# Performance work log

Measured on AMD Instinct MI355X. Metric: run time of the kernel, lower is better.

Reference implementation:

```python
import jax, jax.numpy as jnp
import numpy as np
import math

T = 0.28
EPS = 1e-06
D_MODEL = 1024
N_HEADS = 16
D_K = D_MODEL // N_HEADS


def compute_radius(t, epsilon):
    raw = math.sqrt(4.0 * t * math.log(1.0 / epsilon))
    return max(int(math.ceil(raw * 2.0)), 1)

RADIUS = compute_radius(T, EPS)  # = 8 for t=0.28, eps=1e-6
WIN = RADIUS + 1                 # causal band window: j in [i-RADIUS, i]


def setup_inputs() -> dict:
    key = jax.random.key(0)
    ks = jax.random.split(key, 5)
    B, S = 2, 4096
    x = jax.random.normal(ks[0], (B, S, D_MODEL), dtype=jnp.float32)
    scale = 1.0 / math.sqrt(D_MODEL)
    Wq = jax.random.normal(ks[1], (D_MODEL, D_MODEL), dtype=jnp.float32) * scale
    Wk = jax.random.normal(ks[2], (D_MODEL, D_MODEL), dtype=jnp.float32) * scale
    Wv = jax.random.normal(ks[3], (D_MODEL, D_MODEL), dtype=jnp.float32) * scale
    Wo = jax.random.normal(ks[4], (D_MODEL, D_MODEL), dtype=jnp.float32) * scale
    return {"x": x, "Wq": Wq, "Wk": Wk, "Wv": Wv, "Wo": Wo}


def reference(x, Wq, Wk, Wv, Wo):
    B, S, _ = x.shape

    def split_heads(h):  # (B,S,D) -> (B,H,S,dk)
        return h.reshape(B, S, N_HEADS, D_K).transpose(0, 2, 1, 3)

    q = split_heads(x @ Wq)
    k = split_heads(x @ Wk)
    v = split_heads(x @ Wv)

    # Banded causal attention: token i attends to j in [i-RADIUS, i].
    # This equals the full masked softmax in the torch reference because
    # all out-of-band / non-causal entries are -inf there.
    pos = jnp.arange(S)
    idx = pos[:, None] + jnp.arange(-RADIUS, 1)[None, :]
    valid = idx >= 0                                       # left boundary
    idx_c = jnp.clip(idx, 0, S - 1)

    k_win = k[:, :, idx_c, :]
    v_win = v[:, :, idx_c, :]

    scores = jnp.einsum('bhsd,bhswd->bhsw', q, k_win) / (2.0 * T)
    scores = jnp.where(valid[None, None, :, :], scores, -jnp.inf)
    wts = jax.nn.softmax(scores, axis=-1)
    wts = jnp.nan_to_num(wts, nan=0.0)  # diagonal always valid, but keep parity

    attn = jnp.einsum('bhsw,bhswd->bhsd', wts, v_win)      # (B,H,S,dk)
    attn = attn.transpose(0, 2, 1, 3).reshape(B, S, D_MODEL)
    return attn @ Wo
```

## Files before the change

### kernel.cpp

```cpp
#include <hip/hip_runtime.h>
#include <stdint.h>

constexpr int S_LEN = 4096;
constexpr int DM    = 1024;
constexpr int RAD   = 8;
constexpr float INV2T = 1.7857142857142858f;

constexpr int BM = 128, BN = 128, BK = 64;

typedef _Float16 h8v __attribute__((ext_vector_type(8)));
typedef float f32x4  __attribute__((ext_vector_type(4)));

static __device__ __forceinline__ void gl_lds16(const void* gp, void* lp) {
  auto g = (const __attribute__((address_space(1))) void*)(uintptr_t)gp;
  auto l = (__attribute__((address_space(3))) void*)(uint32_t)(uintptr_t)lp;
  __builtin_amdgcn_global_load_lds(g, l, 16, 0, 0);
}

__global__ __launch_bounds__(256) void sda_cast_kernel(const float* __restrict__ X,
                                                       _Float16* __restrict__ Y) {
  int i = blockIdx.x * 256 + threadIdx.x;
  const float4* x4 = (const float4*)X;
  float4 a = x4[2 * i], b = x4[2 * i + 1];
  float f[8] = {a.x, a.y, a.z, a.w, b.x, b.y, b.z, b.w};
  union { _Float16 h[8]; uint4 v; } o;
#pragma unroll
  for (int j = 0; j < 8; ++j) o.h[j] = (_Float16)f[j];
  ((uint4*)Y)[i] = o.v;
}

__global__ __launch_bounds__(256) void sda_transcast_kernel(
    const float* __restrict__ W0, const float* __restrict__ W1,
    const float* __restrict__ W2, const float* __restrict__ W3,
    _Float16* __restrict__ T0, _Float16* __restrict__ T1,
    _Float16* __restrict__ T2, _Float16* __restrict__ T3) {
  __shared__ float t[32][33];
  const float* W = blockIdx.z == 0 ? W0 : (blockIdx.z == 1 ? W1 : (blockIdx.z == 2 ? W2 : W3));
  _Float16*    T = blockIdx.z == 0 ? T0 : (blockIdx.z == 1 ? T1 : (blockIdx.z == 2 ? T2 : T3));
  int tx = threadIdx.x, ty = threadIdx.y;
  int n0 = blockIdx.x * 32, k0 = blockIdx.y * 32;
#pragma unroll
  for (int i = 0; i < 4; ++i)
    t[ty + 8 * i][tx] = W[(size_t)(k0 + ty + 8 * i) * DM + n0 + tx];
  __syncthreads();
#pragma unroll
  for (int i = 0; i < 4; ++i)
    T[(size_t)(n0 + ty + 8 * i) * DM + k0 + tx] = (_Float16)t[tx][ty + 8 * i];
}

template <bool OUTF16>
__global__ __launch_bounds__(256) void sda_gemm_swz_kernel(
    const _Float16* __restrict__ A, const _Float16* __restrict__ Bt,
    void* __restrict__ C0, void* __restrict__ C1, void* __restrict__ C2) {
  constexpr int Kd = DM;
  __shared__ __align__(16) _Float16 As[BM * BK];
  __shared__ __align__(16) _Float16 Bs[BN * BK];

  int blk = blockIdx.x;
  int xcd = blk & 7, slot = blk >> 3;
  int xt = slot >> 3, ys = slot & 7;
  int yt = (xcd << 3) | ys;
  int m0 = yt * BM, n0 = xt * BN;

  int tid = threadIdx.x, wid = tid >> 6, lane = tid & 63;
  int srow = lane >> 3;
  int sgk = ((lane & 7) ^ (srow & 7)) * 8;
  int wm = (wid >> 1) * 64, wn = (wid & 1) * 64;
  int fm = lane & 15, fc = lane >> 4;

  f32x4 acc[4][4] = {};

  for (int kt = 0; kt < Kd / BK; ++kt) {
    if (kt) __syncthreads();
    int kk = kt * BK;
    int r0 = wid * 32;
#pragma unroll
    for (int i = 0; i < 4; ++i) {
      gl_lds16(A  + (size_t)(m0 + r0 + i * 8 + srow) * Kd + kk + sgk, &As[(r0 + i * 8) * BK]);
      gl_lds16(Bt + (size_t)(n0 + r0 + i * 8 + srow) * Kd + kk + sgk, &Bs[(r0 + i * 8) * BK]);
    }
    __syncthreads();

#pragma unroll
    for (int ks = 0; ks < 2; ++ks) {
      h8v af[4], bfr[4];
#pragma unroll
      for (int i = 0; i < 4; ++i) {
        int row = wm + i * 16 + fm;
        af[i] = *(const h8v*)&As[row * BK + (((ks * 4 + fc) ^ (row & 7)) * 8)];
      }
#pragma unroll
      for (int j = 0; j < 4; ++j) {
        int row = wn + j * 16 + fm;
        bfr[j] = *(const h8v*)&Bs[row * BK + (((ks * 4 + fc) ^ (row & 7)) * 8)];
      }
#pragma unroll
      for (int i = 0; i < 4; ++i)
#pragma unroll
        for (int j = 0; j < 4; ++j)
          acc[i][j] = __builtin_amdgcn_mfma_f32_16x16x32_f16(af[i], bfr[j], acc[i][j], 0, 0, 0);
    }
  }

  int which = n0 >> 10, nc = n0 & 1023;
  void* Cv = which == 0 ? C0 : (which == 1 ? C1 : C2);

  int rr = (lane >> 4) * 4, cc = lane & 15;
#pragma unroll
  for (int i = 0; i < 4; ++i)
#pragma unroll
    for (int j = 0; j < 4; ++j) {
      size_t base = (size_t)(m0 + wm + i * 16 + rr) * DM + (nc + wn + j * 16 + cc);
#pragma unroll
      for (int r = 0; r < 4; ++r) {
        float v = acc[i][j][r];
        if constexpr (OUTF16) ((_Float16*)Cv)[base + (size_t)r * DM] = (_Float16)v;
        else                  ((float*)Cv)[base + (size_t)r * DM] = v;
      }
    }
}

__global__ __launch_bounds__(256) void sda_attn_kernel(
    const _Float16* __restrict__ Q, const _Float16* __restrict__ K,
    const _Float16* __restrict__ V, _Float16* __restrict__ O) {
  constexpr int VS  = 68;
  __shared__ __align__(16) _Float16 qs[64 * 64];
  __shared__ __align__(16) _Float16 ks[80 * 64];
  __shared__ __align__(16) _Float16 vs[96 * VS];
  __shared__ __align__(16) float    scb[4 * 16 * 33];
  __shared__ __align__(16) _Float16 wts[64 * 96];

  int bh = blockIdx.y, b = bh >> 4, h = bh & 15;
  int s0 = blockIdx.x * 64;
  int tid = threadIdx.x;
  size_t headoff = (size_t)b * S_LEN * DM + h * 64;

  for (int idx = tid; idx < 64 * 8; idx += 256) {
    int row = idx >> 3, ch = (idx & 7) * 8;
    *(uint4*)&qs[row * 64 + ch] =
        *(const uint4*)(Q + headoff + (size_t)(s0 + row) * DM + ch);
  }
  for (int idx = tid; idx < 72 * 8; idx += 256) {
    int row = idx >> 3, ch = (idx & 7) * 8;
    int pos = s0 - RAD + row;
    uint4 kv = make_uint4(0, 0, 0, 0), vv = make_uint4(0, 0, 0, 0);
    if (pos >= 0) {
      size_t off = headoff + (size_t)pos * DM + ch;
      kv = *(const uint4*)(K + off);
      vv = *(const uint4*)(V + off);
    }
    *(uint4*)&ks[row * 64 + ch] = kv;
    *(uint2*)&vs[row * VS + ch]     = make_uint2(vv.x, vv.y);
    *(uint2*)&vs[row * VS + ch + 4] = make_uint2(vv.z, vv.w);
  }
  if (tid < 64)
    *(uint4*)&ks[(72 + (tid >> 3)) * 64 + (tid & 7) * 8] = make_uint4(0, 0, 0, 0);
  for (int idx = tid; idx < 24 * 17; idx += 256) {
    int row = 72 + idx / 17, c = (idx % 17) * 4;
    *(uint2*)&vs[row * VS + c] = make_uint2(0, 0);
  }
  for (int idx = tid; idx < 768; idx += 256)
    ((uint4*)wts)[idx] = make_uint4(0, 0, 0, 0);
  __syncthreads();

  int wid = tid >> 6, lane = tid & 63;
  int fm = lane & 15, fkg = (lane >> 4) * 8;
  int rr = (lane >> 4) * 4, cc = lane & 15;

  {
    f32x4 accs[2] = {};
    h8v aq0 = *(const h8v*)&qs[(wid * 16 + fm) * 64 + fkg];
    h8v aq1 = *(const h8v*)&qs[(wid * 16 + fm) * 64 + 32 + fkg];
#pragma unroll
    for (int ti = 0; ti < 2; ++ti) {
      int t = wid + ti;
      h8v bk0 = *(const h8v*)&ks[(t * 16 + fm) * 64 + fkg];
      h8v bk1 = *(const h8v*)&ks[(t * 16 + fm) * 64 + 32 + fkg];
      accs[ti] = __builtin_amdgcn_mfma_f32_16x16x32_f16(aq0, bk0, accs[ti], 0, 0, 0);
      accs[ti] = __builtin_amdgcn_mfma_f32_16x16x32_f16(aq1, bk1, accs[ti], 0, 0, 0);
    }
#pragma unroll
    for (int ti = 0; ti < 2; ++ti)
#pragma unroll
      for (int r = 0; r < 4; ++r)
        scb[wid * 528 + (rr + r) * 33 + ti * 16 + cc] = accs[ti][r];
  }
  __syncthreads();

  if (tid < 64) {
    int r = tid, s = s0 + r;
    const float* my = &scb[(r >> 4) * 528 + (r & 15) * 33 + (r & 15)];
    float e[9], mx = -1e30f;
#pragma unroll
    for (int j = 0; j < 9; ++j) {
      float p = my[j] * INV2T;
      e[j] = (s - RAD + j >= 0) ? p : -1e30f;
      mx = fmaxf(mx, e[j]);
    }
    float se = 0.f;
#pragma unroll
    for (int j = 0; j < 9; ++j) { e[j] = __expf(e[j] - mx); se += e[j]; }
    float inv = 1.f / se;
#pragma unroll
    for (int j = 0; j < 9; ++j)
      wts[r * 96 + r + j] = (_Float16)(e[j] * inv);
  }
  __syncthreads();

  f32x4 acco[4] = {};
#pragma unroll
  for (int step = 0; step < 3; ++step) {
    h8v aw = *(const h8v*)&wts[(wid * 16 + fm) * 96 + step * 32 + fkg];
    int kb = step * 32 + fkg;
#pragma unroll
    for (int t = 0; t < 4; ++t) {
      h8v bv;
#pragma unroll
      for (int j = 0; j < 8; ++j)
        bv[j] = vs[(kb + j) * VS + t * 16 + fm];
      acco[t] = __builtin_amdgcn_mfma_f32_16x16x32_f16(aw, bv, acco[t], 0, 0, 0);
    }
  }
#pragma unroll
  for (int t = 0; t < 4; ++t)
#pragma unroll
    for (int r = 0; r < 4; ++r)
      O[headoff + (size_t)(s0 + wid * 16 + rr + r) * DM + t * 16 + cc] =
          (_Float16)acco[t][r];
}

extern "C" void kernel_launch(void* const* d_in, const int* in_sizes, int n_in,
                              void* d_out, int out_size, void* d_ws, size_t ws_size,
                              hipStream_t stream) {
  (void)in_sizes; (void)n_in; (void)out_size; (void)ws_size;
  const float* x  = (const float*)d_in[0];
  const float* Wq = (const float*)d_in[1];
  const float* Wk = (const float*)d_in[2];
  const float* Wv = (const float*)d_in[3];
  const float* Wo = (const float*)d_in[4];

  char* ws = (char*)d_ws;
  const size_t MB = 1ull << 20;
  _Float16* xh    = (_Float16*)(ws + 0);
  _Float16* WqkvT = (_Float16*)(ws + 16 * MB);
  _Float16* WoT   = (_Float16*)(ws + 22 * MB);
  _Float16* Qh    = (_Float16*)(ws + 24 * MB);
  _Float16* Kh    = (_Float16*)(ws + 40 * MB);
  _Float16* Vh    = (_Float16*)(ws + 56 * MB);
  _Float16* Ah    = (_Float16*)(ws + 72 * MB);

  sda_cast_kernel<<<4096, 256, 0, stream>>>(x, xh);
  sda_transcast_kernel<<<dim3(32, 32, 4), dim3(32, 8), 0, stream>>>(
      Wq, Wk, Wv, Wo,
      WqkvT, WqkvT + (size_t)DM * DM, WqkvT + 2ull * DM * DM, WoT);

  sda_gemm_swz_kernel<true><<<1536, 256, 0, stream>>>(xh, WqkvT, Qh, Kh, Vh);
  sda_attn_kernel<<<dim3(64, 32), 256, 0, stream>>>(Qh, Kh, Vh, Ah);
  sda_gemm_swz_kernel<false><<<512, 256, 0, stream>>>(Ah, WoT, d_out, d_out, d_out);
}
```

Baseline: 190.2 us.

## Fuse prep kernels, narrow Wo GEMM tiles, transpose V in attention LDS

Merges the x cast and the weight transpose-cast into one launch, which saves a kernel launch. Adds a dedicated output-projection GEMM with 128x64 tiles so it runs 1024 blocks instead of 512, giving better CU occupancy on the smaller problem. In the attention kernel, Q fragments are loaded straight from global into registers instead of going through LDS, and V is stored transposed so the PV MFMA operand becomes one vector LDS read instead of eight scalar reads. The risks are smaller tiles lowering data reuse in the Wo GEMM and bank conflicts from the scalar transposed V stores.

```diff
diff --git a/kernel.cpp b/kernel.cpp
--- a/kernel.cpp
+++ b/kernel.cpp
@@ -17,41 +17,43 @@
   __builtin_amdgcn_global_load_lds(g, l, 16, 0, 0);
 }
 
-__global__ __launch_bounds__(256) void sda_cast_kernel(const float* __restrict__ X,
-                                                       _Float16* __restrict__ Y) {
-  int i = blockIdx.x * 256 + threadIdx.x;
-  const float4* x4 = (const float4*)X;
-  float4 a = x4[2 * i], b = x4[2 * i + 1];
-  float f[8] = {a.x, a.y, a.z, a.w, b.x, b.y, b.z, b.w};
-  union { _Float16 h[8]; uint4 v; } o;
-#pragma unroll
-  for (int j = 0; j < 8; ++j) o.h[j] = (_Float16)f[j];
-  ((uint4*)Y)[i] = o.v;
-}
-
-__global__ __launch_bounds__(256) void sda_transcast_kernel(
+__global__ __launch_bounds__(256) void sda_prep_kernel(
+    const float* __restrict__ X, _Float16* __restrict__ XH,
     const float* __restrict__ W0, const float* __restrict__ W1,
     const float* __restrict__ W2, const float* __restrict__ W3,
     _Float16* __restrict__ T0, _Float16* __restrict__ T1,
     _Float16* __restrict__ T2, _Float16* __restrict__ T3) {
   __shared__ float t[32][33];
-  const float* W = blockIdx.z == 0 ? W0 : (blockIdx.z == 1 ? W1 : (blockIdx.z == 2 ? W2 : W3));
-  _Float16*    T = blockIdx.z == 0 ? T0 : (blockIdx.z == 1 ? T1 : (blockIdx.z == 2 ? T2 : T3));
+  int z = blockIdx.z;
   int tx = threadIdx.x, ty = threadIdx.y;
-  int n0 = blockIdx.x * 32, k0 = blockIdx.y * 32;
-#pragma unroll
-  for (int i = 0; i < 4; ++i)
-    t[ty + 8 * i][tx] = W[(size_t)(k0 + ty + 8 * i) * DM + n0 + tx];
-  __syncthreads();
-#pragma unroll
-  for (int i = 0; i < 4; ++i)
-    T[(size_t)(n0 + ty + 8 * i) * DM + k0 + tx] = (_Float16)t[tx][ty + 8 * i];
-}
-
-template <bool OUTF16>
+  if (z < 4) {
+    const float* W = z == 0 ? W0 : (z == 1 ? W1 : (z == 2 ? W2 : W3));
+    _Float16*    T = z == 0 ? T0 : (z == 1 ? T1 : (z == 2 ? T2 : T3));
+    int n0 = blockIdx.x * 32, k0 = blockIdx.y * 32;
+#pragma unroll
+    for (int i = 0; i < 4; ++i)
+      t[ty + 8 * i][tx] = W[(size_t)(k0 + ty + 8 * i) * DM + n0 + tx];
+    __syncthreads();
+#pragma unroll
+    for (int i = 0; i < 4; ++i)
+      T[(size_t)(n0 + ty + 8 * i) * DM + k0 + tx] = (_Float16)t[tx][ty + 8 * i];
+  } else {
+    int blk = (z - 4) * 1024 + blockIdx.y * 32 + blockIdx.x;
+    int i = blk * 256 + ty * 32 + tx;
+    const float4* x4 = (const float4*)X;
+    float4 a = x4[2 * i], b = x4[2 * i + 1];
+    float f[8] = {a.x, a.y, a.z, a.w, b.x, b.y, b.z, b.w};
+    union { _Float16 h[8]; uint4 v; } o;
+#pragma unroll
+    for (int j = 0; j < 8; ++j) o.h[j] = (_Float16)f[j];
+    ((uint4*)XH)[i] = o.v;
+  }
+}
+
 __global__ __launch_bounds__(256) void sda_gemm_swz_kernel(
     const _Float16* __restrict__ A, const _Float16* __restrict__ Bt,
-    void* __restrict__ C0, void* __restrict__ C1, void* __restrict__ C2) {
+    _Float16* __restrict__ C0, _Float16* __restrict__ C1,
+    _Float16* __restrict__ C2) {
   constexpr int Kd = DM;
   __shared__ __align__(16) _Float16 As[BM * BK];
   __shared__ __align__(16) _Float16 Bs[BN * BK];
@@ -103,7 +105,7 @@
   }
 
   int which = n0 >> 10, nc = n0 & 1023;
-  void* Cv = which == 0 ? C0 : (which == 1 ? C1 : C2);
+  _Float16* Cv = which == 0 ? C0 : (which == 1 ? C1 : C2);
 
   int rr = (lane >> 4) * 4, cc = lane & 15;
 #pragma unroll
@@ -112,21 +114,84 @@
     for (int j = 0; j < 4; ++j) {
       size_t base = (size_t)(m0 + wm + i * 16 + rr) * DM + (nc + wn + j * 16 + cc);
 #pragma unroll
-      for (int r = 0; r < 4; ++r) {
-        float v = acc[i][j][r];
-        if constexpr (OUTF16) ((_Float16*)Cv)[base + (size_t)r * DM] = (_Float16)v;
-        else                  ((float*)Cv)[base + (size_t)r * DM] = v;
+      for (int r = 0; r < 4; ++r)
+        Cv[base + (size_t)r * DM] = (_Float16)acc[i][j][r];
+    }
+}
+
+__global__ __launch_bounds__(256) void sda_gemm_wo_kernel(
+    const _Float16* __restrict__ A, const _Float16* __restrict__ Bt,
+    float* __restrict__ C) {
+  constexpr int Kd = DM, BN2 = 64;
+  __shared__ __align__(16) _Float16 As[BM * BK];
+  __shared__ __align__(16) _Float16 Bs[BN2 * BK];
+
+  int blk = blockIdx.x;
+  int xcd = blk & 7, slot = blk >> 3;
+  int xt = slot >> 3, ys = slot & 7;
+  int yt = (xcd << 3) | ys;
+  int m0 = yt * BM, n0 = xt * BN2;
+
+  int tid = threadIdx.x, wid = tid >> 6, lane = tid & 63;
+  int srow = lane >> 3;
+  int sgk = ((lane & 7) ^ (srow & 7)) * 8;
+  int wm = (wid >> 1) * 64, wn = (wid & 1) * 32;
+  int fm = lane & 15, fc = lane >> 4;
+
+  f32x4 acc[4][2] = {};
+
+  for (int kt = 0; kt < Kd / BK; ++kt) {
+    if (kt) __syncthreads();
+    int kk = kt * BK;
+#pragma unroll
+    for (int i = 0; i < 4; ++i)
+      gl_lds16(A + (size_t)(m0 + wid * 32 + i * 8 + srow) * Kd + kk + sgk,
+               &As[(wid * 32 + i * 8) * BK]);
+#pragma unroll
+    for (int i = 0; i < 2; ++i)
+      gl_lds16(Bt + (size_t)(n0 + wid * 16 + i * 8 + srow) * Kd + kk + sgk,
+               &Bs[(wid * 16 + i * 8) * BK]);
+    __syncthreads();
+
+#pragma unroll
+    for (int ks = 0; ks < 2; ++ks) {
+      h8v af[4], bfr[2];
+#pragma unroll
+      for (int i = 0; i < 4; ++i) {
+        int row = wm + i * 16 + fm;
+        af[i] = *(const h8v*)&As[row * BK + (((ks * 4 + fc) ^ (row & 7)) * 8)];
       }
+#pragma unroll
+      for (int j = 0; j < 2; ++j) {
+        int row = wn + j * 16 + fm;
+        bfr[j] = *(const h8v*)&Bs[row * BK + (((ks * 4 + fc) ^ (row & 7)) * 8)];
+      }
+#pragma unroll
+      for (int i = 0; i < 4; ++i)
+#pragma unroll
+        for (int j = 0; j < 2; ++j)
+          acc[i][j] = __builtin_amdgcn_mfma_f32_16x16x32_f16(af[i], bfr[j], acc[i][j], 0, 0, 0);
+    }
+  }
+
+  int rr = (lane >> 4) * 4, cc = lane & 15;
+#pragma unroll
+  for (int i = 0; i < 4; ++i)
+#pragma unroll
+    for (int j = 0; j < 2; ++j) {
+      size_t base = (size_t)(m0 + wm + i * 16 + rr) * DM + (n0 + wn + j * 16 + cc);
+#pragma unroll
+      for (int r = 0; r < 4; ++r)
+        C[base + (size_t)r * DM] = acc[i][j][r];
     }
 }
 
 __global__ __launch_bounds__(256) void sda_attn_kernel(
     const _Float16* __restrict__ Q, const _Float16* __restrict__ K,
     const _Float16* __restrict__ V, _Float16* __restrict__ O) {
-  constexpr int VS  = 68;
-  __shared__ __align__(16) _Float16 qs[64 * 64];
+  constexpr int VTS = 104;
   __shared__ __align__(16) _Float16 ks[80 * 64];
-  __shared__ __align__(16) _Float16 vs[96 * VS];
+  __shared__ __align__(16) _Float16 vst[64 * VTS];
   __shared__ __align__(16) float    scb[4 * 16 * 33];
   __shared__ __align__(16) _Float16 wts[64 * 96];
 
@@ -135,42 +200,42 @@
   int tid = threadIdx.x;
   size_t headoff = (size_t)b * S_LEN * DM + h * 64;
 
-  for (int idx = tid; idx < 64 * 8; idx += 256) {
-    int row = idx >> 3, ch = (idx & 7) * 8;
-    *(uint4*)&qs[row * 64 + ch] =
-        *(const uint4*)(Q + headoff + (size_t)(s0 + row) * DM + ch);
-  }
+  int wid = tid >> 6, lane = tid & 63;
+  int fm = lane & 15, fkg = (lane >> 4) * 8;
+  int rr = (lane >> 4) * 4, cc = lane & 15;
+
+  const _Float16* qrow = Q + headoff + (size_t)(s0 + wid * 16 + fm) * DM;
+  h8v aq0 = *(const h8v*)(qrow + fkg);
+  h8v aq1 = *(const h8v*)(qrow + 32 + fkg);
+
   for (int idx = tid; idx < 72 * 8; idx += 256) {
     int row = idx >> 3, ch = (idx & 7) * 8;
     int pos = s0 - RAD + row;
-    uint4 kv = make_uint4(0, 0, 0, 0), vv = make_uint4(0, 0, 0, 0);
-    if (pos >= 0) {
-      size_t off = headoff + (size_t)pos * DM + ch;
-      kv = *(const uint4*)(K + off);
-      vv = *(const uint4*)(V + off);
-    }
+    uint4 kv = make_uint4(0, 0, 0, 0);
+    if (pos >= 0) kv = *(const uint4*)(K + headoff + (size_t)pos * DM + ch);
     *(uint4*)&ks[row * 64 + ch] = kv;
-    *(uint2*)&vs[row * VS + ch]     = make_uint2(vv.x, vv.y);
-    *(uint2*)&vs[row * VS + ch + 4] = make_uint2(vv.z, vv.w);
+  }
+  for (int idx = tid; idx < 72 * 8; idx += 256) {
+    int row = idx % 72, chb = (idx / 72) * 8;
+    int pos = s0 - RAD + row;
+    uint4 vv = make_uint4(0, 0, 0, 0);
+    if (pos >= 0) vv = *(const uint4*)(V + headoff + (size_t)pos * DM + chb);
+    union { uint4 v; _Float16 hh[8]; } u; u.v = vv;
+#pragma unroll
+    for (int d = 0; d < 8; ++d) vst[(chb + d) * VTS + row] = u.hh[d];
   }
   if (tid < 64)
     *(uint4*)&ks[(72 + (tid >> 3)) * 64 + (tid & 7) * 8] = make_uint4(0, 0, 0, 0);
-  for (int idx = tid; idx < 24 * 17; idx += 256) {
-    int row = 72 + idx / 17, c = (idx % 17) * 4;
-    *(uint2*)&vs[row * VS + c] = make_uint2(0, 0);
+  for (int idx = tid; idx < 64 * 6; idx += 256) {
+    int dim = idx / 6, p = idx % 6;
+    *(uint2*)&vst[dim * VTS + 72 + p * 4] = make_uint2(0, 0);
   }
   for (int idx = tid; idx < 768; idx += 256)
     ((uint4*)wts)[idx] = make_uint4(0, 0, 0, 0);
   __syncthreads();
 
-  int wid = tid >> 6, lane = tid & 63;
-  int fm = lane & 15, fkg = (lane >> 4) * 8;
-  int rr = (lane >> 4) * 4, cc = lane & 15;
-
   {
     f32x4 accs[2] = {};
-    h8v aq0 = *(const h8v*)&qs[(wid * 16 + fm) * 64 + fkg];
-    h8v aq1 = *(const h8v*)&qs[(wid * 16 + fm) * 64 + 32 + fkg];
 #pragma unroll
     for (int ti = 0; ti < 2; ++ti) {
       int t = wid + ti;
@@ -214,10 +279,7 @@
     int kb = step * 32 + fkg;
 #pragma unroll
     for (int t = 0; t < 4; ++t) {
-      h8v bv;
-#pragma unroll
-      for (int j = 0; j < 8; ++j)
-        bv[j] = vs[(kb + j) * VS + t * 16 + fm];
+      h8v bv = *(const h8v*)&vst[(t * 16 + fm) * VTS + kb];
       acco[t] = __builtin_amdgcn_mfma_f32_16x16x32_f16(aw, bv, acco[t], 0, 0, 0);
     }
   }
@@ -249,12 +311,11 @@
   _Float16* Vh    = (_Float16*)(ws + 56 * MB);
   _Float16* Ah    = (_Float16*)(ws + 72 * MB);
 
-  sda_cast_kernel<<<4096, 256, 0, stream>>>(x, xh);
-  sda_transcast_kernel<<<dim3(32, 32, 4), dim3(32, 8), 0, stream>>>(
-      Wq, Wk, Wv, Wo,
+  sda_prep_kernel<<<dim3(32, 32, 8), dim3(32, 8), 0, stream>>>(
+      x, xh, Wq, Wk, Wv, Wo,
       WqkvT, WqkvT + (size_t)DM * DM, WqkvT + 2ull * DM * DM, WoT);
 
-  sda_gemm_swz_kernel<true><<<1536, 256, 0, stream>>>(xh, WqkvT, Qh, Kh, Vh);
+  sda_gemm_swz_kernel<<<1536, 256, 0, stream>>>(xh, WqkvT, Qh, Kh, Vh);
   sda_attn_kernel<<<dim3(64, 32), 256, 0, stream>>>(Qh, Kh, Vh, Ah);
-  sda_gemm_swz_kernel<false><<<512, 256, 0, stream>>>(Ah, WoT, d_out, d_out, d_out);
-}
+  sda_gemm_wo_kernel<<<1024, 256, 0, stream>>>(Ah, WoT, (float*)d_out);
+}
```

New measurement: 189.9 us. Within noise of the previous version (-0.2%).
